# Performance work log

Measured on AMD Instinct MI355X. Metric: run time of the kernel, lower is better.

Reference implementation:

```python
import jax, jax.numpy as jnp
import numpy as np

N = 50000   # nodes
E = 800000  # edges (before self-loops)
IN = 128; H = 4; C = 32; HC = H * C; OUT = 47
EPS = 1e-16  # PyG softmax denominator eps
NEG_SLOPE = 0.2


def setup_inputs() -> dict:
    key = jax.random.key(0)
    ks = jax.random.split(key, 20)
    g = lambda k, shape, s=0.1: (jax.random.normal(k, shape, dtype=jnp.float32) * s)
    inp = {}
    inp["x"] = jax.random.normal(ks[0], (N, IN), dtype=jnp.float32)
    inp["edge_index"] = jax.random.randint(ks[1], (2, E), 0, N, dtype=jnp.int32)
    # layer 0: GATConv(IN -> H*C, concat=True) + skip Linear(IN -> HC)
    inp["lin_w0"] = g(ks[2], (IN, HC)); inp["att_src0"] = g(ks[3], (H, C)); inp["att_dst0"] = g(ks[4], (H, C))
    inp["bias0"] = g(ks[5], (HC,)); inp["skip_w0"] = g(ks[6], (IN, HC)); inp["skip_b0"] = g(ks[7], (HC,))
    # layer 1: GATConv(HC -> H*C, concat=True) + skip Linear(HC -> HC)
    inp["lin_w1"] = g(ks[8], (HC, HC)); inp["att_src1"] = g(ks[9], (H, C)); inp["att_dst1"] = g(ks[10], (H, C))
    inp["bias1"] = g(ks[11], (HC,)); inp["skip_w1"] = g(ks[12], (HC, HC)); inp["skip_b1"] = g(ks[13], (HC,))
    # layer 2: GATConv(HC -> OUT, heads=H, concat=False) + skip Linear(HC -> OUT)
    inp["lin_w2"] = g(ks[14], (HC, H * OUT)); inp["att_src2"] = g(ks[15], (H, OUT)); inp["att_dst2"] = g(ks[16], (H, OUT))
    inp["bias2"] = g(ks[17], (OUT,)); inp["skip_w2"] = g(ks[18], (HC, OUT)); inp["skip_b2"] = g(ks[19], (OUT,))
    return inp


def _gat_conv(x, src, dst, lin_w, att_src, att_dst, bias, concat):
    """PyG GATConv (self-loops already appended to src/dst)."""
    h, c = att_src.shape
    n = x.shape[0]
    xh = (x @ lin_w).reshape(n, h, c)                      # [N, H, C]
    a_src = jnp.einsum('nhc,hc->nh', xh, att_src)          # [N, H]
    a_dst = jnp.einsum('nhc,hc->nh', xh, att_dst)          # [N, H]
    e = a_src[src] + a_dst[dst]                            # [E', H]
    e = jax.nn.leaky_relu(e, NEG_SLOPE)
    # segment softmax over incoming edges per destination node
    m = jax.ops.segment_max(e, dst, num_segments=n)        # [N, H]
    ex = jnp.exp(e - m[dst])
    s = jax.ops.segment_sum(ex, dst, num_segments=n)       # [N, H]
    alpha = ex / (s[dst] + EPS)                            # [E', H]
    out = jax.ops.segment_sum(xh[src] * alpha[:, :, None], dst, num_segments=n)  # [N, H, C]
    out = out.reshape(n, h * c) if concat else out.mean(axis=1)
    return out + bias


def reference(x, edge_index, lin_w0, att_src0, att_dst0, bias0, skip_w0, skip_b0,
              lin_w1, att_src1, att_dst1, bias1, skip_w1, skip_b1,
              lin_w2, att_src2, att_dst2, bias2, skip_w2, skip_b2):
    n = x.shape[0]
    loop = jnp.arange(n, dtype=edge_index.dtype)
    src = jnp.concatenate([edge_index[0], loop])
    dst = jnp.concatenate([edge_index[1], loop])
    # layer 0 (+ skip, ELU; dropout is identity at inference)
    x = _gat_conv(x, src, dst, lin_w0, att_src0, att_dst0, bias0, True) + x @ skip_w0 + skip_b0
    x = jax.nn.elu(x)
    # layer 1
    x = _gat_conv(x, src, dst, lin_w1, att_src1, att_dst1, bias1, True) + x @ skip_w1 + skip_b1
    x = jax.nn.elu(x)
    # layer 2 (concat=False -> head mean), no activation
    x = _gat_conv(x, src, dst, lin_w2, att_src2, att_dst2, bias2, False) + x @ skip_w2 + skip_b2
    return x
```

## Files before the change

kernel.cpp:

```cpp
#include <hip/hip_runtime.h>
#include <math.h>
#include <type_traits>

#define KD 128
#define HC 128
#define NF2 188
#define NF2PB 192
#define OUTC 47

typedef __attribute__((ext_vector_type(8))) __bf16 bf16x8;
typedef __attribute__((ext_vector_type(4))) float f32x4;
typedef __attribute__((ext_vector_type(2))) float f32x2;

#ifdef __has_builtin
#if __has_builtin(__builtin_amdgcn_cvt_pk_f32_fp8)
#define HAVE_CVT_FP8_DEC 1
#endif
#if __has_builtin(__builtin_amdgcn_cvt_pk_fp8_f32)
#define HAVE_CVT_FP8_ENC 1
#endif
#endif

__device__ inline float bfhi_to_f(unsigned int u) {
    union { unsigned int u; float f; } c; c.u = u & 0xFFFF0000u; return c.f;
}
__device__ inline float bflo_to_f(unsigned int u) {
    union { unsigned int u; float f; } c; c.u = u << 16; return c.f;
}
__device__ inline unsigned short f_to_bfu(float f) {
    return __builtin_bit_cast(unsigned short, (__bf16)f);
}
__device__ inline unsigned int pk_bf(float a, float b) {
    return (unsigned int)f_to_bfu(a) | ((unsigned int)f_to_bfu(b) << 16);
}

#ifndef HAVE_CVT_FP8_DEC
__device__ inline float fp8_to_f32_b(unsigned int b) {
    int e = (b >> 3) & 15, m = b & 7;
    float v = e ? ldexpf((float)(8 + m), e - 10) : ldexpf((float)m, -9);
    return (b & 0x80) ? -v : v;
}
#endif
__device__ inline void fp8x4_dec(unsigned int q, float& a, float& b, float& c, float& d) {
#ifdef HAVE_CVT_FP8_DEC
    f32x2 lo = __builtin_amdgcn_cvt_pk_f32_fp8((int)q, false);
    f32x2 hi = __builtin_amdgcn_cvt_pk_f32_fp8((int)q, true);
    a = lo[0]; b = lo[1]; c = hi[0]; d = hi[1];
#else
    a = fp8_to_f32_b(q & 0xFF); b = fp8_to_f32_b((q >> 8) & 0xFF);
    c = fp8_to_f32_b((q >> 16) & 0xFF); d = fp8_to_f32_b((q >> 24) & 0xFF);
#endif
}
__device__ inline unsigned char f32_to_fp8(float v) {
#ifdef HAVE_CVT_FP8_ENC
    return (unsigned char)(__builtin_amdgcn_cvt_pk_fp8_f32(v, v, 0, false) & 0xFF);
#else
    unsigned u = __builtin_bit_cast(unsigned, v);
    unsigned s = (u >> 24) & 0x80;
    float a = fabsf(v);
    if (a < 0.0009765625f) return (unsigned char)s;
    if (a >= 448.f) return (unsigned char)(s | 0x7E);
    int e; float m = frexpf(a, &e);
    int E = e - 1 + 7;
    int mi = (int)rintf(m * 16.f);
    if (mi == 16) { mi = 8; ++E; if (E >= 16) return (unsigned char)(s | 0x7E); }
    if (E <= 0) {
        int q = (int)rintf(a * 512.f); if (q > 7) q = 7;
        return (unsigned char)(s | q);
    }
    return (unsigned char)(s | (E << 3) | (mi - 8));
#endif
}
__device__ inline float fp8dot(unsigned int q, float4 al, float acc) {
    float a, b, c, d;
    fp8x4_dec(q, a, b, c, d);
    return acc + al.x * a + al.y * b + al.z * c + al.w * d;
}

__global__ void count_kernel(const int* __restrict__ dst, int* deg, int e) {
    int t = blockIdx.x * blockDim.x + threadIdx.x;
    int base = t * 8;
    if (base + 7 < e) {
        int4 d0 = *(const int4*)(dst + base);
        int4 d1 = *(const int4*)(dst + base + 4);
        atomicAdd(&deg[d0.x], 1); atomicAdd(&deg[d0.y], 1);
        atomicAdd(&deg[d0.z], 1); atomicAdd(&deg[d0.w], 1);
        atomicAdd(&deg[d1.x], 1); atomicAdd(&deg[d1.y], 1);
        atomicAdd(&deg[d1.z], 1); atomicAdd(&deg[d1.w], 1);
    } else {
        for (int k = base; k < e; ++k) atomicAdd(&deg[dst[k]], 1);
    }
}

__global__ __launch_bounds__(256) void scan_base_kernel(
    int* __restrict__ deg, int* counter,
    int* __restrict__ row_ptr, int* __restrict__ fill, int* __restrict__ col, int n) {
    int i = blockIdx.x * 256 + threadIdx.x;
    int v = (i < n) ? (deg[i] + 1) : 0;
    int lane = threadIdx.x & 63, w = threadIdx.x >> 6;
    int incl = v;
#pragma unroll
    for (int off = 1; off < 64; off <<= 1) {
        int u = __shfl_up(incl, off, 64);
        if (lane >= off) incl += u;
    }
    __shared__ int wsum[4];
    __shared__ int base_sh;
    if (lane == 63) wsum[w] = incl;
    __syncthreads();
    if (threadIdx.x == 0)
        base_sh = atomicAdd(counter, wsum[0] + wsum[1] + wsum[2] + wsum[3]);
    int woff = 0;
    for (int k = 0; k < w; ++k) woff += wsum[k];
    __syncthreads();
    int excl = base_sh + woff + incl - v;
    if (i < n) {
        row_ptr[i] = excl;
        col[excl] = i;
        fill[i] = excl + 1;
        deg[i] = v;
    }
}

__global__ void fill_kernel(const int* __restrict__ ei, int* fill, int* col, int e) {
    int t = blockIdx.x * blockDim.x + threadIdx.x;
    int base = t * 8;
    if (base + 7 < e) {
        int4 s0 = *(const int4*)(ei + base);
        int4 s1 = *(const int4*)(ei + base + 4);
        int4 d0 = *(const int4*)(ei + e + base);
        int4 d1 = *(const int4*)(ei + e + base + 4);
        int p0 = atomicAdd(&fill[d0.x], 1);
        int p1 = atomicAdd(&fill[d0.y], 1);
        int p2 = atomicAdd(&fill[d0.z], 1);
        int p3 = atomicAdd(&fill[d0.w], 1);
        int p4 = atomicAdd(&fill[d1.x], 1);
        int p5 = atomicAdd(&fill[d1.y], 1);
        int p6 = atomicAdd(&fill[d1.z], 1);
        int p7 = atomicAdd(&fill[d1.w], 1);
        col[p0] = s0.x; col[p1] = s0.y; col[p2] = s0.z; col[p3] = s0.w;
        col[p4] = s1.x; col[p5] = s1.y; col[p6] = s1.z; col[p7] = s1.w;
    } else {
        for (int k = base; k < e; ++k) {
            int pos = atomicAdd(&fill[ei[e + k]], 1);
            col[pos] = ei[k];
        }
    }
}

template <typename AT, typename SKT, int NLIN, int NSK, int TR>
__global__ __launch_bounds__(256) void gemm_fused_kernel(
    const AT* __restrict__ A,
    const float* __restrict__ B0, void* __restrict__ out0, int N0, int ldc0,
    const float* __restrict__ B1, const float* __restrict__ bias1,
    SKT* __restrict__ out1, int N1, int M) {
    __shared__ __bf16 As[64][136];
    __shared__ __bf16 Bs[64][136];
    int tid = threadIdx.x;
    int m0 = blockIdx.x * 64;

#pragma unroll
    for (int rep = 0; rep < 4; ++rep) {
        int idx = tid + rep * 256;
        int row = idx >> 4, seg = idx & 15;
        int gm = m0 + row;
        bf16x8 v = {};
        if (gm < M) {
            if constexpr (std::is_same<AT, float>::value) {
                const float* p = A + gm * KD + seg * 8;
                float4 f0 = *(const float4*)p;
                float4 f1 = *(const float4*)(p + 4);
                v[0] = (__bf16)f0.x; v[1] = (__bf16)f0.y; v[2] = (__bf16)f0.z; v[3] = (__bf16)f0.w;
                v[4] = (__bf16)f1.x; v[5] = (__bf16)f1.y; v[6] = (__bf16)f1.z; v[7] = (__bf16)f1.w;
            } else {
                v = *(const bf16x8*)(A + gm * KD + seg * 8);
            }
        }
        *(bf16x8*)&As[row][seg * 8] = v;
    }
    __syncthreads();

    int w = tid >> 6, lane = tid & 63;
    int lr = lane & 15, quad = lane >> 4;

#pragma unroll
    for (int t = 0; t < NLIN + NSK; ++t) {
        bool second = t >= NLIN;
        const float* B = second ? B1 : B0;
        int N = second ? N1 : N0;
        int n0 = (second ? (t - NLIN) : t) * 64;
        if (t) __syncthreads();
#pragma unroll
        for (int rep = 0; rep < 4; ++rep) {
            int idx = tid + rep * 256;
            int n = idx & 63, seg = idx >> 6;
            bf16x8 v = {};
            if (n0 + n < N) {
#pragma unroll
                for (int i = 0; i < 8; ++i) v[i] = (__bf16)B[(seg * 8 + i) * N + n0 + n];
            }
            *(bf16x8*)&Bs[n][seg * 8] = v;
        }
        __syncthreads();

        f32x4 acc[4] = {};
#pragma unroll
        for (int kc = 0; kc < 128; kc += 32) {
            bf16x8 a0 = *(const bf16x8*)&As[w * 16 + lr][kc + quad * 8];
            bf16x8 b0 = *(const bf16x8*)&Bs[lr][kc + quad * 8];
            bf16x8 b1 = *(const bf16x8*)&Bs[16 + lr][kc + quad * 8];
            bf16x8 b2 = *(const bf16x8*)&Bs[32 + lr][kc + quad * 8];
            bf16x8 b3 = *(const bf16x8*)&Bs[48 + lr][kc + quad * 8];
            acc[0] = __builtin_amdgcn_mfma_f32_16x16x32_bf16(a0, b0, acc[0], 0, 0, 0);
            acc[1] = __builtin_amdgcn_mfma_f32_16x16x32_bf16(a0, b1, acc[1], 0, 0, 0);
            acc[2] = __builtin_amdgcn_mfma_f32_16x16x32_bf16(a0, b2, acc[2], 0, 0, 0);
            acc[3] = __builtin_amdgcn_mfma_f32_16x16x32_bf16(a0, b3, acc[3], 0, 0, 0);
        }
#pragma unroll
        for (int c = 0; c < 4; ++c) {
#pragma unroll
            for (int reg = 0; reg < 4; ++reg) {
                int row = m0 + w * 16 + quad * 4 + reg;
                int colg = n0 + c * 16 + lr;
                if (row < M && colg < N) {
                    float v = acc[c][reg];
                    if (second) {
                        if (bias1) v += bias1[colg];
                        out1[row * N + colg] = (SKT)v;
                    } else if (TR) {
                        int h = (colg * 1395) >> 16;
                        ((unsigned char*)out0)[row * ldc0 + (colg - 47 * h) * 4 + h] =
                            f32_to_fp8(v);
                    } else {
                        ((__bf16*)out0)[row * ldc0 + colg] = (__bf16)v;
                    }
                }
            }
        }
    }
}

__global__ __launch_bounds__(256) void att_kernel(
    const __bf16* __restrict__ xh, const float* __restrict__ att_s,
    const float* __restrict__ att_d, float* __restrict__ a_src,
    float* __restrict__ a_dst, int n) {
    int tid = blockIdx.x * 256 + threadIdx.x;
    int node = tid >> 4;
    int l16 = threadIdx.x & 15;
    if (node >= n) return;
    uint4 q = ((const uint4*)xh)[node * 16 + l16];
    int f0 = l16 * 8;
    float4 as0 = *(const float4*)(att_s + f0);
    float4 as1 = *(const float4*)(att_s + f0 + 4);
    float4 ad0 = *(const float4*)(att_d + f0);
    float4 ad1 = *(const float4*)(att_d + f0 + 4);
    float x0 = bflo_to_f(q.x), x1 = bfhi_to_f(q.x);
    float x2 = bflo_to_f(q.y), x3 = bfhi_to_f(q.y);
    float x4 = bflo_to_f(q.z), x5 = bfhi_to_f(q.z);
    float x6 = bflo_to_f(q.w), x7 = bfhi_to_f(q.w);
    float hs = x0 * as0.x + x1 * as0.y + x2 * as0.z + x3 * as0.w
             + x4 * as1.x + x5 * as1.y + x6 * as1.z + x7 * as1.w;
    float hd = x0 * ad0.x + x1 * ad0.y + x2 * ad0.z + x3 * ad0.w
             + x4 * ad1.x + x5 * ad1.y + x6 * ad1.z + x7 * ad1.w;
    hs += __shfl_xor(hs, 1, 64); hs += __shfl_xor(hs, 2, 64);
    hd += __shfl_xor(hd, 1, 64); hd += __shfl_xor(hd, 2, 64);
    if ((l16 & 3) == 0) {
        int h = l16 >> 2;
        a_src[node * 4 + h] = hs;
        a_dst[node * 4 + h] = hd;
    }
}

__global__ __launch_bounds__(256) void att2_kernel(
    const unsigned char* __restrict__ xh8, const float* __restrict__ att_s,
    const float* __restrict__ att_d, float* __restrict__ a_src,
    float* __restrict__ a_dst, int n) {
    int node = (blockIdx.x * 256 + threadIdx.x) >> 6;
    int lane = threadIdx.x & 63;
    if (node >= n) return;
    float ps0 = 0.f, ps1 = 0.f, ps2 = 0.f, ps3 = 0.f;
    float pd0 = 0.f, pd1 = 0.f, pd2 = 0.f, pd3 = 0.f;
    if (lane < 47) {
        unsigned int q = ((const unsigned int*)(xh8 + node * NF2PB))[lane];
        float x0, x1, x2, x3;
        fp8x4_dec(q, x0, x1, x2, x3);
        ps0 = x0 * att_s[lane];       ps1 = x1 * att_s[47 + lane];
        ps2 = x2 * att_s[94 + lane];  ps3 = x3 * att_s[141 + lane];
        pd0 = x0 * att_d[lane];       pd1 = x1 * att_d[47 + lane];
        pd2 = x2 * att_d[94 + lane];  pd3 = x3 * att_d[141 + lane];
    }
#pragma unroll
    for (int off = 1; off <= 32; off <<= 1) {
        ps0 += __shfl_xor(ps0, off, 64); ps1 += __shfl_xor(ps1, off, 64);
        ps2 += __shfl_xor(ps2, off, 64); ps3 += __shfl_xor(ps3, off, 64);
        pd0 += __shfl_xor(pd0, off, 64); pd1 += __shfl_xor(pd1, off, 64);
        pd2 += __shfl_xor(pd2, off, 64); pd3 += __shfl_xor(pd3, off, 64);
    }
    if (lane < 4) {
        float vs = (lane == 0) ? ps0 : (lane == 1) ? ps1 : (lane == 2) ? ps2 : ps3;
        float vd = (lane == 0) ? pd0 : (lane == 1) ? pd1 : (lane == 2) ? pd2 : pd3;
        a_src[node * 4 + lane] = vs;
        a_dst[node * 4 + lane] = vd;
    }
}

template <int MODE>
__global__ __launch_bounds__(256) void agg_kernel(
    const void* __restrict__ xhp, const float* __restrict__ a_src,
    const float* __restrict__ a_dst, const void* __restrict__ skipp,
    const float* __restrict__ bias, const int* __restrict__ row_ptr,
    const int* __restrict__ deg, const int* __restrict__ col,
    void* __restrict__ outp, int n) {
    __shared__ float s_af[4][64][4];
    __shared__ int s_j[4][64];
    int w = threadIdx.x >> 6;
    int lane = threadIdx.x & 63;
    int node = (blockIdx.x << 2) + w;
    bool active = node < n;
    int node_c = active ? node : 0;
    int start = row_ptr[node_c];
    int end = start + (active ? deg[node_c] : 0);
    float4 ad4 = *(const float4*)(a_dst + 4 * node_c);
    float adh[4] = {ad4.x, ad4.y, ad4.z, ad4.w};

    int e0 = start + lane;
    bool ok0 = e0 < end;
    int jcap = ok0 ? col[e0] : 0;
    float evc[4];
    {
        float4 as4 = *(const float4*)(a_src + 4 * jcap);
        float v0 = as4.x + adh[0]; v0 = v0 > 0.f ? v0 : 0.2f * v0;
        float v1 = as4.y + adh[1]; v1 = v1 > 0.f ? v1 : 0.2f * v1;
        float v2 = as4.z + adh[2]; v2 = v2 > 0.f ? v2 : 0.2f * v2;
        float v3 = as4.w + adh[3]; v3 = v3 > 0.f ? v3 : 0.2f * v3;
        evc[0] = ok0 ? __expf(v0) : 0.f;
        evc[1] = ok0 ? __expf(v1) : 0.f;
        evc[2] = ok0 ? __expf(v2) : 0.f;
        evc[3] = ok0 ? __expf(v3) : 0.f;
    }
    float s[4] = {evc[0], evc[1], evc[2], evc[3]};
    for (int e = e0 + 64; e < end; e += 64) {
        int j = col[e];
        float4 as4 = *(const float4*)(a_src + 4 * j);
        float ev[4] = {as4.x + adh[0], as4.y + adh[1], as4.z + adh[2], as4.w + adh[3]};
#pragma unroll
        for (int h = 0; h < 4; ++h) {
            float v = ev[h] > 0.f ? ev[h] : 0.2f * ev[h];
            s[h] += __expf(v);
        }
    }
#pragma unroll
    for (int off = 32; off >= 1; off >>= 1)
#pragma unroll
        for (int h = 0; h < 4; ++h) s[h] += __shfl_xor(s[h], off, 64);
    float inv[4];
#pragma unroll
    for (int h = 0; h < 4; ++h) inv[h] = 1.f / (s[h] + 1e-16f);

    int half = lane >> 5, fl = lane & 31, myh2 = fl >> 3;
    bool lv = lane < 47;
    float acc0 = 0.f, acc1 = 0.f, acc2 = 0.f, acc3 = 0.f;
    const uint2* xb2 = (const uint2*)xhp;
    const unsigned int* x8 = (const unsigned int*)xhp;

    auto run_chunk = [&](int cnt) {
        int t = 0;
        if (MODE == 0) {
            for (; t + 7 < cnt; t += 8) {
                int ja = s_j[w][t + half], jb = s_j[w][t + 2 + half];
                int jc = s_j[w][t + 4 + half], jd = s_j[w][t + 6 + half];
                uint2 qa = xb2[(ja << 5) + fl];
                uint2 qb = xb2[(jb << 5) + fl];
                uint2 qc = xb2[(jc << 5) + fl];
                uint2 qd = xb2[(jd << 5) + fl];
                float aa = s_af[w][t + half][myh2];
                float ab = s_af[w][t + 2 + half][myh2];
                float ac = s_af[w][t + 4 + half][myh2];
                float ad = s_af[w][t + 6 + half][myh2];
                acc0 += aa * bflo_to_f(qa.x); acc1 += aa * bfhi_to_f(qa.x);
                acc2 += aa * bflo_to_f(qa.y); acc3 += aa * bfhi_to_f(qa.y);
                acc0 += ab * bflo_to_f(qb.x); acc1 += ab * bfhi_to_f(qb.x);
                acc2 += ab * bflo_to_f(qb.y); acc3 += ab * bfhi_to_f(qb.y);
                acc0 += ac * bflo_to_f(qc.x); acc1 += ac * bfhi_to_f(qc.x);
                acc2 += ac * bflo_to_f(qc.y); acc3 += ac * bfhi_to_f(qc.y);
                acc0 += ad * bflo_to_f(qd.x); acc1 += ad * bfhi_to_f(qd.x);
                acc2 += ad * bflo_to_f(qd.y); acc3 += ad * bfhi_to_f(qd.y);
            }
            for (; t + 3 < cnt; t += 4) {
                int ja = s_j[w][t + half], jb = s_j[w][t + 2 + half];
                uint2 qa = xb2[(ja << 5) + fl];
                uint2 qb = xb2[(jb << 5) + fl];
                float aa = s_af[w][t + half][myh2];
                float ab = s_af[w][t + 2 + half][myh2];
                acc0 += aa * bflo_to_f(qa.x); acc1 += aa * bfhi_to_f(qa.x);
                acc2 += aa * bflo_to_f(qa.y); acc3 += aa * bfhi_to_f(qa.y);
                acc0 += ab * bflo_to_f(qb.x); acc1 += ab * bfhi_to_f(qb.x);
                acc2 += ab * bflo_to_f(qb.y); acc3 += ab * bfhi_to_f(qb.y);
            }
            for (; t + 1 < cnt; t += 2) {
                int j = s_j[w][t + half];
                uint2 q = xb2[(j << 5) + fl];
                float a = s_af[w][t + half][myh2];
                acc0 += a * bflo_to_f(q.x); acc1 += a * bfhi_to_f(q.x);
                acc2 += a * bflo_to_f(q.y); acc3 += a * bfhi_to_f(q.y);
            }
            for (; t < cnt; ++t) {
                int j = s_j[w][t];
                uint2 q = xb2[(j << 5) + fl];
                float a = (half == 0) ? s_af[w][t][myh2] : 0.f;
                acc0 += a * bflo_to_f(q.x); acc1 += a * bfhi_to_f(q.x);
                acc2 += a * bflo_to_f(q.y); acc3 += a * bfhi_to_f(q.y);
            }
        } else {
            for (; t + 7 < cnt; t += 8) {
                unsigned int q0 = lv ? x8[s_j[w][t] * 48 + lane] : 0u;
                unsigned int q1 = lv ? x8[s_j[w][t + 1] * 48 + lane] : 0u;
                unsigned int q2 = lv ? x8[s_j[w][t + 2] * 48 + lane] : 0u;
                unsigned int q3 = lv ? x8[s_j[w][t + 3] * 48 + lane] : 0u;
                unsigned int q4 = lv ? x8[s_j[w][t + 4] * 48 + lane] : 0u;
                unsigned int q5 = lv ? x8[s_j[w][t + 5] * 48 + lane] : 0u;
                unsigned int q6 = lv ? x8[s_j[w][t + 6] * 48 + lane] : 0u;
                unsigned int q7 = lv ? x8[s_j[w][t + 7] * 48 + lane] : 0u;
                acc0 = fp8dot(q0, *(const float4*)&s_af[w][t][0], acc0);
                acc0 = fp8dot(q1, *(const float4*)&s_af[w][t + 1][0], acc0);
                acc0 = fp8dot(q2, *(const float4*)&s_af[w][t + 2][0], acc0);
                acc0 = fp8dot(q3, *(const float4*)&s_af[w][t + 3][0], acc0);
                acc0 = fp8dot(q4, *(const float4*)&s_af[w][t + 4][0], acc0);
                acc0 = fp8dot(q5, *(const float4*)&s_af[w][t + 5][0], acc0);
                acc0 = fp8dot(q6, *(const float4*)&s_af[w][t + 6][0], acc0);
                acc0 = fp8dot(q7, *(const float4*)&s_af[w][t + 7][0], acc0);
            }
            for (; t + 3 < cnt; t += 4) {
                unsigned int q0 = lv ? x8[s_j[w][t] * 48 + lane] : 0u;
                unsigned int q1 = lv ? x8[s_j[w][t + 1] * 48 + lane] : 0u;
                unsigned int q2 = lv ? x8[s_j[w][t + 2] * 48 + lane] : 0u;
                unsigned int q3 = lv ? x8[s_j[w][t + 3] * 48 + lane] : 0u;
                acc0 = fp8dot(q0, *(const float4*)&s_af[w][t][0], acc0);
                acc0 = fp8dot(q1, *(const float4*)&s_af[w][t + 1][0], acc0);
                acc0 = fp8dot(q2, *(const float4*)&s_af[w][t + 2][0], acc0);
                acc0 = fp8dot(q3, *(const float4*)&s_af[w][t + 3][0], acc0);
            }
            for (; t < cnt; ++t) {
                unsigned int q = lv ? x8[s_j[w][t] * 48 + lane] : 0u;
                acc0 = fp8dot(q, *(const float4*)&s_af[w][t][0], acc0);
            }
        }
    };

    {
        float al[4];
#pragma unroll
        for (int h = 0; h < 4; ++h) al[h] = evc[h] * inv[h];
        s_j[w][lane] = jcap;
        *(float4*)&s_af[w][lane][0] = make_float4(al[0], al[1], al[2], al[3]);
        int cnt = end - start; if (cnt > 64) cnt = 64;
        run_chunk(cnt);
    }
    for (int base = start + 64; base < end; base += 64) {
        int e = base + lane;
        bool ok = e < end;
        int jv = ok ? col[e] : 0;
        float4 as4 = *(const float4*)(a_src + 4 * jv);
        float asv[4] = {as4.x, as4.y, as4.z, as4.w};
        float al[4];
#pragma unroll
        for (int h = 0; h < 4; ++h) {
            float ev = asv[h] + adh[h];
            ev = ev > 0.f ? ev : 0.2f * ev;
            al[h] = ok ? __expf(ev) * inv[h] : 0.f;
        }
        s_j[w][lane] = jv;
        *(float4*)&s_af[w][lane][0] = make_float4(al[0], al[1], al[2], al[3]);
        int cnt = end - base; if (cnt > 64) cnt = 64;
        run_chunk(cnt);
    }

    if constexpr (MODE == 0) {
        acc0 += __shfl_xor(acc0, 32, 64);
        acc1 += __shfl_xor(acc1, 32, 64);
        acc2 += __shfl_xor(acc2, 32, 64);
        acc3 += __shfl_xor(acc3, 32, 64);
        if (active && half == 0) {
            float4 bb = *(const float4*)(bias + 4 * fl);
            uint2 skq = ((const uint2*)skipp)[(node << 5) + fl];
            float v0 = acc0 + bb.x + bflo_to_f(skq.x);
            float v1 = acc1 + bb.y + bfhi_to_f(skq.x);
            float v2 = acc2 + bb.z + bflo_to_f(skq.y);
            float v3 = acc3 + bb.w + bfhi_to_f(skq.y);
            v0 = v0 > 0.f ? v0 : (__expf(v0) - 1.f);
            v1 = v1 > 0.f ? v1 : (__expf(v1) - 1.f);
            v2 = v2 > 0.f ? v2 : (__expf(v2) - 1.f);
            v3 = v3 > 0.f ? v3 : (__expf(v3) - 1.f);
            uint2 o = make_uint2(pk_bf(v0, v1), pk_bf(v2, v3));
            ((uint2*)outp)[(node << 5) + fl] = o;
        }
    } else {
        if (active && lane < OUTC) {
            const float* skip = (const float*)skipp;
            float v = acc0 * 0.25f + bias[lane] + skip[node * OUTC + lane];
            ((float*)outp)[node * OUTC + lane] = v;
        }
    }
}

extern "C" void kernel_launch(void* const* d_in, const int* in_sizes, int n_in,
                              void* d_out, int out_size, void* d_ws, size_t ws_size,
                              hipStream_t stream) {
    const float* x        = (const float*)d_in[0];
    const int*   ei       = (const int*)d_in[1];
    const float* lin_w0   = (const float*)d_in[2];
    const float* att_src0 = (const float*)d_in[3];
    const float* att_dst0 = (const float*)d_in[4];
    const float* bias0    = (const float*)d_in[5];
    const float* skip_w0  = (const float*)d_in[6];
    const float* skip_b0  = (const float*)d_in[7];
    const float* lin_w1   = (const float*)d_in[8];
    const float* att_src1 = (const float*)d_in[9];
    const float* att_dst1 = (const float*)d_in[10];
    const float* bias1    = (const float*)d_in[11];
    const float* skip_w1  = (const float*)d_in[12];
    const float* skip_b1  = (const float*)d_in[13];
    const float* lin_w2   = (const float*)d_in[14];
    const float* att_src2 = (const float*)d_in[15];
    const float* att_dst2 = (const float*)d_in[16];
    const float* bias2    = (const float*)d_in[17];
    const float* skip_w2  = (const float*)d_in[18];
    const float* skip_b2  = (const float*)d_in[19];
    float* out = (float*)d_out;

    const int N = in_sizes[0] / KD;
    const int E = in_sizes[1] / 2;
    const int ET_ = E + N;

    char* ws = (char*)d_ws;
    size_t off = 0;
    auto alloc = [&](size_t bytes) -> void* {
        void* p = ws + off;
        off = (off + bytes + 255) & ~(size_t)255;
        return p;
    };
    void*   xh      = alloc((size_t)N * HC * 2 + 256);
    __bf16* buf_bf  = (__bf16*)alloc((size_t)N * HC * 2);
    void*   skipbuf = alloc((size_t)N * HC * 4);
    float* a_src    = (float*)alloc((size_t)N * 4 * 4);
    float* a_dst    = (float*)alloc((size_t)N * 4 * 4);
    int* deg        = (int*)alloc((size_t)N * 4);
    int* row_ptr    = (int*)alloc((size_t)N * 4);
    int* fill       = (int*)alloc((size_t)N * 4);
    int* col        = (int*)alloc((size_t)ET_ * 4);
    int* counter    = (int*)alloc(256);

    hipMemsetAsync(deg, 0, (size_t)N * 4, stream);
    hipMemsetAsync(counter, 0, 4, stream);
    count_kernel<<<(E / 8 + 255) / 256, 256, 0, stream>>>(ei + E, deg, E);
    scan_base_kernel<<<(N + 255) / 256, 256, 0, stream>>>(deg, counter, row_ptr, fill, col, N);
    fill_kernel<<<(E / 8 + 255) / 256, 256, 0, stream>>>(ei, fill, col, E);

    dim3 blk(256);
    int mblocks = (N + 63) / 64;
    int wave_blocks = (N + 3) / 4;
    int att_blocks = (N * 16 + 255) / 256;

    gemm_fused_kernel<float, __bf16, 2, 2, 0><<<mblocks, blk, 0, stream>>>(
        x, lin_w0, xh, HC, HC, skip_w0, skip_b0, (__bf16*)skipbuf, HC, N);
    att_kernel<<<att_blocks, blk, 0, stream>>>((const __bf16*)xh, att_src0, att_dst0,
                                               a_src, a_dst, N);
    agg_kernel<0><<<wave_blocks, blk, 0, stream>>>(xh, a_src, a_dst, skipbuf, bias0,
                                                   row_ptr, deg, col, buf_bf, N);
    gemm_fused_kernel<__bf16, __bf16, 2, 2, 0><<<mblocks, blk, 0, stream>>>(
        buf_bf, lin_w1, xh, HC, HC, skip_w1, skip_b1, (__bf16*)skipbuf, HC, N);
    att_kernel<<<att_blocks, blk, 0, stream>>>((const __bf16*)xh, att_src1, att_dst1,
                                               a_src, a_dst, N);
    agg_kernel<0><<<wave_blocks, blk, 0, stream>>>(xh, a_src, a_dst, skipbuf, bias1,
                                                   row_ptr, deg, col, buf_bf, N);
    gemm_fused_kernel<__bf16, float, 3, 1, 1><<<mblocks, blk, 0, stream>>>(
        buf_bf, lin_w2, xh, NF2, NF2PB, skip_w2, skip_b2, (float*)skipbuf, OUTC, N);
    att2_kernel<<<wave_blocks, blk, 0, stream>>>((const unsigned char*)xh, att_src2,
                                                 att_dst2, a_src, a_dst, N);
    agg_kernel<1><<<wave_blocks, blk, 0, stream>>>(xh, a_src, a_dst, skipbuf, bias2,
                                                   row_ptr, deg, col, out, N);
}
```

Measured before the change: 403.2 us.

## Pre-transpose weights to bf16 and use packed bf16 dot2 in aggregation

Adds a one-off kernel that converts and transposes all linear and skip weights into a bf16 [n][k] buffer, so the GEMM kernels read B fragments straight from global memory instead of staging strided fp32 loads through shared memory with extra barriers. In the MODE 0 aggregation, attention weights for edge pairs are packed into bf16 pairs, and neighbor features are byte-permuted so each v_dot2_f32_bf16 handles two edges per instruction. This halves the FMA and unpack work in the gather loop at the cost of rounding alpha to bf16. It also adds a small extra launch.

```diff
diff --git a/kernel.cpp b/kernel.cpp
--- a/kernel.cpp
+++ b/kernel.cpp
@@ -32,6 +32,13 @@
 }
 __device__ inline unsigned int pk_bf(float a, float b) {
     return (unsigned int)f_to_bfu(a) | ((unsigned int)f_to_bfu(b) << 16);
+}
+
+__device__ inline void dot2bf(float& acc, unsigned int x, unsigned int a) {
+    asm("v_dot2_f32_bf16 %0, %1, %2, %0" : "+v"(acc) : "v"(x), "v"(a));
+}
+__device__ inline unsigned int permb(unsigned int hi, unsigned int lo, unsigned int sel) {
+    return __builtin_amdgcn_perm(hi, lo, sel);
 }
 
 #ifndef HAVE_CVT_FP8_DEC
@@ -148,14 +155,31 @@
     }
 }
 
+__global__ __launch_bounds__(256) void prep_w_kernel(
+    const float* __restrict__ lw0, const float* __restrict__ sw0,
+    const float* __restrict__ lw1, const float* __restrict__ sw1,
+    const float* __restrict__ lw2, const float* __restrict__ sw2,
+    __bf16* __restrict__ bt) {
+    int idx = blockIdx.x * 256 + threadIdx.x;
+    int buf = idx >> 15;
+    int r = idx & 32767;
+    int n = r >> 7, k = r & 127;
+    float v = 0.f;
+    if (buf == 0) v = (n < 128) ? lw0[k * 128 + n] : sw0[k * 128 + n - 128];
+    else if (buf == 1) v = (n < 128) ? lw1[k * 128 + n] : sw1[k * 128 + n - 128];
+    else {
+        if (n < 188) v = lw2[k * 188 + n];
+        else if (n >= 192 && n < 239) v = sw2[k * 47 + n - 192];
+    }
+    bt[idx] = (__bf16)v;
+}
+
 template <typename AT, typename SKT, int NLIN, int NSK, int TR>
 __global__ __launch_bounds__(256) void gemm_fused_kernel(
-    const AT* __restrict__ A,
-    const float* __restrict__ B0, void* __restrict__ out0, int N0, int ldc0,
-    const float* __restrict__ B1, const float* __restrict__ bias1,
-    SKT* __restrict__ out1, int N1, int M) {
+    const AT* __restrict__ A, const __bf16* __restrict__ Bt,
+    void* __restrict__ out0, int N0, int ldc0,
+    const float* __restrict__ bias1, SKT* __restrict__ out1, int N1, int M) {
     __shared__ __bf16 As[64][136];
-    __shared__ __bf16 Bs[64][136];
     int tid = threadIdx.x;
     int m0 = blockIdx.x * 64;
 
@@ -186,31 +210,18 @@
 #pragma unroll
     for (int t = 0; t < NLIN + NSK; ++t) {
         bool second = t >= NLIN;
-        const float* B = second ? B1 : B0;
         int N = second ? N1 : N0;
         int n0 = (second ? (t - NLIN) : t) * 64;
-        if (t) __syncthreads();
-#pragma unroll
-        for (int rep = 0; rep < 4; ++rep) {
-            int idx = tid + rep * 256;
-            int n = idx & 63, seg = idx >> 6;
-            bf16x8 v = {};
-            if (n0 + n < N) {
-#pragma unroll
-                for (int i = 0; i < 8; ++i) v[i] = (__bf16)B[(seg * 8 + i) * N + n0 + n];
-            }
-            *(bf16x8*)&Bs[n][seg * 8] = v;
-        }
-        __syncthreads();
+        const __bf16* bbase = Bt + ((t * 64 + lr) << 7) + quad * 8;
 
         f32x4 acc[4] = {};
 #pragma unroll
         for (int kc = 0; kc < 128; kc += 32) {
             bf16x8 a0 = *(const bf16x8*)&As[w * 16 + lr][kc + quad * 8];
-            bf16x8 b0 = *(const bf16x8*)&Bs[lr][kc + quad * 8];
-            bf16x8 b1 = *(const bf16x8*)&Bs[16 + lr][kc + quad * 8];
-            bf16x8 b2 = *(const bf16x8*)&Bs[32 + lr][kc + quad * 8];
-            bf16x8 b3 = *(const bf16x8*)&Bs[48 + lr][kc + quad * 8];
+            bf16x8 b0 = *(const bf16x8*)(bbase + kc);
+            bf16x8 b1 = *(const bf16x8*)(bbase + (16 << 7) + kc);
+            bf16x8 b2 = *(const bf16x8*)(bbase + (32 << 7) + kc);
+            bf16x8 b3 = *(const bf16x8*)(bbase + (48 << 7) + kc);
             acc[0] = __builtin_amdgcn_mfma_f32_16x16x32_bf16(a0, b0, acc[0], 0, 0, 0);
             acc[1] = __builtin_amdgcn_mfma_f32_16x16x32_bf16(a0, b1, acc[1], 0, 0, 0);
             acc[2] = __builtin_amdgcn_mfma_f32_16x16x32_bf16(a0, b2, acc[2], 0, 0, 0);
@@ -225,7 +236,7 @@
                 if (row < M && colg < N) {
                     float v = acc[c][reg];
                     if (second) {
-                        if (bias1) v += bias1[colg];
+                        v += bias1[colg];
                         out1[row * N + colg] = (SKT)v;
                     } else if (TR) {
                         int h = (colg * 1395) >> 16;
@@ -312,6 +323,7 @@
     const int* __restrict__ deg, const int* __restrict__ col,
     void* __restrict__ outp, int n) {
     __shared__ float s_af[4][64][4];
+    __shared__ unsigned s_ap[4][32][4];
     __shared__ int s_j[4][64];
     int w = threadIdx.x >> 6;
     int lane = threadIdx.x & 63;
@@ -364,54 +376,39 @@
     const unsigned int* x8 = (const unsigned int*)xhp;
 
     auto run_chunk = [&](int cnt) {
-        int t = 0;
-        if (MODE == 0) {
-            for (; t + 7 < cnt; t += 8) {
-                int ja = s_j[w][t + half], jb = s_j[w][t + 2 + half];
-                int jc = s_j[w][t + 4 + half], jd = s_j[w][t + 6 + half];
-                uint2 qa = xb2[(ja << 5) + fl];
-                uint2 qb = xb2[(jb << 5) + fl];
-                uint2 qc = xb2[(jc << 5) + fl];
-                uint2 qd = xb2[(jd << 5) + fl];
-                float aa = s_af[w][t + half][myh2];
-                float ab = s_af[w][t + 2 + half][myh2];
-                float ac = s_af[w][t + 4 + half][myh2];
-                float ad = s_af[w][t + 6 + half][myh2];
-                acc0 += aa * bflo_to_f(qa.x); acc1 += aa * bfhi_to_f(qa.x);
-                acc2 += aa * bflo_to_f(qa.y); acc3 += aa * bfhi_to_f(qa.y);
-                acc0 += ab * bflo_to_f(qb.x); acc1 += ab * bfhi_to_f(qb.x);
-                acc2 += ab * bflo_to_f(qb.y); acc3 += ab * bfhi_to_f(qb.y);
-                acc0 += ac * bflo_to_f(qc.x); acc1 += ac * bfhi_to_f(qc.x);
-                acc2 += ac * bflo_to_f(qc.y); acc3 += ac * bfhi_to_f(qc.y);
-                acc0 += ad * bflo_to_f(qd.x); acc1 += ad * bfhi_to_f(qd.x);
-                acc2 += ad * bflo_to_f(qd.y); acc3 += ad * bfhi_to_f(qd.y);
-            }
-            for (; t + 3 < cnt; t += 4) {
-                int ja = s_j[w][t + half], jb = s_j[w][t + 2 + half];
-                uint2 qa = xb2[(ja << 5) + fl];
-                uint2 qb = xb2[(jb << 5) + fl];
-                float aa = s_af[w][t + half][myh2];
-                float ab = s_af[w][t + 2 + half][myh2];
-                acc0 += aa * bflo_to_f(qa.x); acc1 += aa * bfhi_to_f(qa.x);
-                acc2 += aa * bflo_to_f(qa.y); acc3 += aa * bfhi_to_f(qa.y);
-                acc0 += ab * bflo_to_f(qb.x); acc1 += ab * bfhi_to_f(qb.x);
-                acc2 += ab * bflo_to_f(qb.y); acc3 += ab * bfhi_to_f(qb.y);
-            }
-            for (; t + 1 < cnt; t += 2) {
-                int j = s_j[w][t + half];
-                uint2 q = xb2[(j << 5) + fl];
-                float a = s_af[w][t + half][myh2];
-                acc0 += a * bflo_to_f(q.x); acc1 += a * bfhi_to_f(q.x);
-                acc2 += a * bflo_to_f(q.y); acc3 += a * bfhi_to_f(q.y);
-            }
-            for (; t < cnt; ++t) {
-                int j = s_j[w][t];
-                uint2 q = xb2[(j << 5) + fl];
-                float a = (half == 0) ? s_af[w][t][myh2] : 0.f;
-                acc0 += a * bflo_to_f(q.x); acc1 += a * bfhi_to_f(q.x);
-                acc2 += a * bflo_to_f(q.y); acc3 += a * bfhi_to_f(q.y);
+        if constexpr (MODE == 0) {
+            int npair = (cnt + 1) >> 1;
+            int p = half;
+            for (; p + 2 < npair; p += 4) {
+                int2 j0 = *(const int2*)&s_j[w][2 * p];
+                int2 j1 = *(const int2*)&s_j[w][2 * p + 4];
+                unsigned ap0 = s_ap[w][p][myh2];
+                unsigned ap1 = s_ap[w][p + 2][myh2];
+                uint2 qa0 = xb2[(j0.x << 5) + fl];
+                uint2 qb0 = xb2[(j0.y << 5) + fl];
+                uint2 qa1 = xb2[(j1.x << 5) + fl];
+                uint2 qb1 = xb2[(j1.y << 5) + fl];
+                dot2bf(acc0, permb(qb0.x, qa0.x, 0x05040100u), ap0);
+                dot2bf(acc1, permb(qb0.x, qa0.x, 0x07060302u), ap0);
+                dot2bf(acc2, permb(qb0.y, qa0.y, 0x05040100u), ap0);
+                dot2bf(acc3, permb(qb0.y, qa0.y, 0x07060302u), ap0);
+                dot2bf(acc0, permb(qb1.x, qa1.x, 0x05040100u), ap1);
+                dot2bf(acc1, permb(qb1.x, qa1.x, 0x07060302u), ap1);
+                dot2bf(acc2, permb(qb1.y, qa1.y, 0x05040100u), ap1);
+                dot2bf(acc3, permb(qb1.y, qa1.y, 0x07060302u), ap1);
+            }
+            for (; p < npair; p += 2) {
+                int2 j0 = *(const int2*)&s_j[w][2 * p];
+                unsigned ap0 = s_ap[w][p][myh2];
+                uint2 qa0 = xb2[(j0.x << 5) + fl];
+                uint2 qb0 = xb2[(j0.y << 5) + fl];
+                dot2bf(acc0, permb(qb0.x, qa0.x, 0x05040100u), ap0);
+                dot2bf(acc1, permb(qb0.x, qa0.x, 0x07060302u), ap0);
+                dot2bf(acc2, permb(qb0.y, qa0.y, 0x05040100u), ap0);
+                dot2bf(acc3, permb(qb0.y, qa0.y, 0x07060302u), ap0);
             }
         } else {
+            int t = 0;
             for (; t + 7 < cnt; t += 8) {
                 unsigned int q0 = lv ? x8[s_j[w][t] * 48 + lane] : 0u;
                 unsigned int q1 = lv ? x8[s_j[w][t + 1] * 48 + lane] : 0u;
@@ -452,7 +449,19 @@
 #pragma unroll
         for (int h = 0; h < 4; ++h) al[h] = evc[h] * inv[h];
         s_j[w][lane] = jcap;
-        *(float4*)&s_af[w][lane][0] = make_float4(al[0], al[1], al[2], al[3]);
+        if constexpr (MODE == 0) {
+            float o0 = __shfl_xor(al[0], 1, 64);
+            float o1 = __shfl_xor(al[1], 1, 64);
+            float o2 = __shfl_xor(al[2], 1, 64);
+            float o3 = __shfl_xor(al[3], 1, 64);
+            if (!(lane & 1)) {
+                uint4 pk = make_uint4(pk_bf(al[0], o0), pk_bf(al[1], o1),
+                                      pk_bf(al[2], o2), pk_bf(al[3], o3));
+                *(uint4*)&s_ap[w][lane >> 1][0] = pk;
+            }
+        } else {
+            *(float4*)&s_af[w][lane][0] = make_float4(al[0], al[1], al[2], al[3]);
+        }
         int cnt = end - start; if (cnt > 64) cnt = 64;
         run_chunk(cnt);
     }
@@ -470,7 +479,19 @@
             al[h] = ok ? __expf(ev) * inv[h] : 0.f;
         }
         s_j[w][lane] = jv;
-        *(float4*)&s_af[w][lane][0] = make_float4(al[0], al[1], al[2], al[3]);
+        if constexpr (MODE == 0) {
+            float o0 = __shfl_xor(al[0], 1, 64);
+            float o1 = __shfl_xor(al[1], 1, 64);
+            float o2 = __shfl_xor(al[2], 1, 64);
+            float o3 = __shfl_xor(al[3], 1, 64);
+            if (!(lane & 1)) {
+                uint4 pk = make_uint4(pk_bf(al[0], o0), pk_bf(al[1], o1),
+                                      pk_bf(al[2], o2), pk_bf(al[3], o3));
+                *(uint4*)&s_ap[w][lane >> 1][0] = pk;
+            }
+        } else {
+            *(float4*)&s_af[w][lane][0] = make_float4(al[0], al[1], al[2], al[3]);
+        }
         int cnt = end - base; if (cnt > 64) cnt = 64;
         run_chunk(cnt);
     }
@@ -549,6 +570,10 @@
     int* fill       = (int*)alloc((size_t)N * 4);
     int* col        = (int*)alloc((size_t)ET_ * 4);
     int* counter    = (int*)alloc(256);
+    __bf16* Bt      = (__bf16*)alloc((size_t)3 * 256 * 128 * 2);
+
+    prep_w_kernel<<<384, 256, 0, stream>>>(lin_w0, skip_w0, lin_w1, skip_w1,
+                                           lin_w2, skip_w2, Bt);
 
     hipMemsetAsync(deg, 0, (size_t)N * 4, stream);
     hipMemsetAsync(counter, 0, 4, stream);
@@ -562,19 +587,19 @@
     int att_blocks = (N * 16 + 255) / 256;
 
     gemm_fused_kernel<float, __bf16, 2, 2, 0><<<mblocks, blk, 0, stream>>>(
-        x, lin_w0, xh, HC, HC, skip_w0, skip_b0, (__bf16*)skipbuf, HC, N);
+        x, Bt, xh, HC, HC, skip_b0, (__bf16*)skipbuf, HC, N);
     att_kernel<<<att_blocks, blk, 0, stream>>>((const __bf16*)xh, att_src0, att_dst0,
                                                a_src, a_dst, N);
     agg_kernel<0><<<wave_blocks, blk, 0, stream>>>(xh, a_src, a_dst, skipbuf, bias0,
                                                    row_ptr, deg, col, buf_bf, N);
     gemm_fused_kernel<__bf16, __bf16, 2, 2, 0><<<mblocks, blk, 0, stream>>>(
-        buf_bf, lin_w1, xh, HC, HC, skip_w1, skip_b1, (__bf16*)skipbuf, HC, N);
+        buf_bf, Bt + 32768, xh, HC, HC, skip_b1, (__bf16*)skipbuf, HC, N);
     att_kernel<<<att_blocks, blk, 0, stream>>>((const __bf16*)xh, att_src1, att_dst1,
                                                a_src, a_dst, N);
     agg_kernel<0><<<wave_blocks, blk, 0, stream>>>(xh, a_src, a_dst, skipbuf, bias1,
                                                    row_ptr, deg, col, buf_bf, N);
     gemm_fused_kernel<__bf16, float, 3, 1, 1><<<mblocks, blk, 0, stream>>>(
-        buf_bf, lin_w2, xh, NF2, NF2PB, skip_w2, skip_b2, (float*)skipbuf, OUTC, N);
+        buf_bf, Bt + 65536, xh, NF2, NF2PB, skip_b2, (float*)skipbuf, OUTC, N);
     att2_kernel<<<wave_blocks, blk, 0, stream>>>((const unsigned char*)xh, att_src2,
                                                  att_dst2, a_src, a_dst, N);
     agg_kernel<1><<<wave_blocks, blk, 0, stream>>>(xh, a_src, a_dst, skipbuf, bias2,
```

Result: slower. 456.5 us (+13.2%).
